# Optimization experiments

Hardware: AMD Instinct MI355X
Metric: run time of the kernel (lower is better)

## Reference

```python
import jax, jax.numpy as jnp
import numpy as np

B, C, H, W = 8, 256, 64, 64
NUM_HEADS = 4


def setup_inputs() -> dict:
    key = jax.random.key(0)
    ks = jax.random.split(key, 6)
    s = 0.02  # small init scale for 1x1 conv weights
    return {
        "x": jax.random.normal(ks[0], (B, C, H, W), jnp.float32),
        "cproj": jax.random.normal(ks[1], (B, C, H, W), jnp.float32),
        "wq": jax.random.normal(ks[2], (C, C), jnp.float32) * s,
        "bq": jnp.zeros((C,), jnp.float32),
        "wkv": jax.random.normal(ks[3], (2 * C, C), jnp.float32) * s,
        "bkv": jnp.zeros((2 * C,), jnp.float32),
        "wo": jax.random.normal(ks[4], (C, C), jnp.float32) * s,  # zero_module in torch; random here for a meaningful baseline
        "bo": jnp.zeros((C,), jnp.float32),
    }


def reference(x, cproj, wq, bq, wkv, bkv, wo, bo):
    Bb, Cc, Hh, Ww = x.shape
    N = Hh * Ww
    h = NUM_HEADS
    d = Cc // h
    scale = 1.0 / jnp.sqrt(jnp.sqrt(jnp.asarray(Cc, jnp.float32)))

    xf = x.reshape(Bb, Cc, N)
    cf = cproj.reshape(Bb, Cc, N)

    # 1x1 convs == channel matmuls
    Q = jnp.einsum('oc,bcn->bon', wq, xf) + bq[None, :, None]           # (B,C,N)
    KV = jnp.einsum('oc,bcn->bon', wkv, cf) + bkv[None, :, None]        # (B,2C,N)
    K, V = KV[:, :Cc], KV[:, Cc:]

    # softmax over channel-dim-within-head for q, over spatial N for k
    q = jax.nn.softmax(Q.reshape(Bb, h, d, N) * scale, axis=2).reshape(Bb, Cc, N)
    k = jax.nn.softmax(K.reshape(Bb, h, d, N), axis=3).reshape(Bb, Cc, N)

    # linear-attention: (B,C,C) context, then project back to N — note heads are mixed, per original bmm
    context = jnp.einsum('bcn,bdn->bcd', k, V)
    out = jnp.einsum('bcd,bdn->bcn', context, q)

    out = jnp.einsum('oc,bcn->bon', wo, out) + bo[None, :, None]
    return out.reshape(Bb, Cc, Hh, Ww)
```

## Files before the change

### kernel.cpp

```cpp
#include <hip/hip_runtime.h>

#define B_ 8
#define C_ 256
#define N_ 4096
#define NSPLIT 16

typedef float f32x4 __attribute__((ext_vector_type(4)));
typedef __bf16 bf16x8 __attribute__((ext_vector_type(8)));
typedef unsigned short u16x8 __attribute__((ext_vector_type(8)));
typedef unsigned short u16x4 __attribute__((ext_vector_type(4)));

__device__ __forceinline__ unsigned short f2bf(float f) {
  unsigned u = __float_as_uint(f);
  u += 0x7fff + ((u >> 16) & 1);
  return (unsigned short)(u >> 16);
}

__device__ __forceinline__ f32x4 mfma16(bf16x8 a, bf16x8 b, f32x4 c) {
  return __builtin_amdgcn_mfma_f32_16x16x32_bf16(a, b, c, 0, 0, 0);
}

typedef __attribute__((address_space(1))) const void* gvp;
typedef __attribute__((address_space(3))) void* lvp;
__device__ __forceinline__ void gld16(const void* g, void* l) {
  __builtin_amdgcn_global_load_lds((gvp)g, (lvp)l, 16, 0, 0);
}

template <int ROWS>
__device__ __forceinline__ void stage(unsigned short* lds, const unsigned short* g,
                                      int ld, int w, int lane) {
  const int r8 = lane >> 3;
  const int ce = ((lane & 7) ^ r8) << 3;
  const unsigned short* gp = g + (size_t)(w * (ROWS / 4) + r8) * ld + ce;
  unsigned short* lp = lds + w * (ROWS / 4) * 64;
#pragma unroll
  for (int i = 0; i < ROWS / 32; i++)
    gld16(gp + (size_t)(i * 8) * ld, lp + i * 512);
}

__device__ __forceinline__ bf16x8 frag(const unsigned short* lds, int row, int kc) {
  return *(const bf16x8*)(lds + row * 64 + ((kc ^ (row & 7)) << 3));
}

__device__ __forceinline__ void loadB(float4* pbv, const float* src, int ld,
                                      int n0, int kt, int w, int lane) {
  const int nf = lane & 15, kg = lane >> 4;
  const float* sp = src + (size_t)(kt * 64 + w * 16 + kg * 4) * ld + n0 + 4 * nf;
#pragma unroll
  for (int i = 0; i < 4; i++) pbv[i] = *(const float4*)(sp + (size_t)i * ld);
}
__device__ __forceinline__ void writeB(unsigned short* Bs, const float4* pbv,
                                       int w, int lane) {
  const int nf = lane & 15, kg = lane >> 4;
  const int k0 = w * 16 + kg * 4;
#pragma unroll
  for (int j = 0; j < 4; j++) {
    u16x4 o = (u16x4){f2bf(((const float*)&pbv[0])[j]), f2bf(((const float*)&pbv[1])[j]),
                      f2bf(((const float*)&pbv[2])[j]), f2bf(((const float*)&pbv[3])[j])};
    *(u16x4*)&Bs[(4 * nf + j) * 68 + k0] = o;
  }
}
__device__ __forceinline__ bf16x8 fragB(const unsigned short* Bs, int n, int k8) {
  union { u16x4 q[2]; bf16x8 b; } u;
  const unsigned short* p = Bs + n * 68 + k8 * 8;
  u.q[0] = *(const u16x4*)p;
  u.q[1] = *(const u16x4*)(p + 4);
  return u.b;
}

__global__ __launch_bounds__(256) void castw(
    const float* __restrict__ wq, const float* __restrict__ wkv,
    const float* __restrict__ wo, unsigned short* __restrict__ wqb,
    unsigned short* __restrict__ wkvb, unsigned short* __restrict__ wob) {
  int i = (blockIdx.x * 256 + threadIdx.x) * 4;
  const float* src;
  unsigned short* dst;
  int off;
  if (i < 65536) { src = wq; dst = wqb; off = i; }
  else if (i < 196608) { src = wkv; dst = wkvb; off = i - 65536; }
  else { src = wo; dst = wob; off = i - 196608; }
  float4 v = *(const float4*)(src + off);
  *(u16x4*)(dst + off) = (u16x4){f2bf(v.x), f2bf(v.y), f2bf(v.z), f2bf(v.w)};
}

__device__ __forceinline__ void qproj_body(
    unsigned short* As, unsigned short* Bs, const unsigned short* __restrict__ wqb,
    const float* __restrict__ x, const float* __restrict__ bq,
    unsigned short* __restrict__ qT, int b, int n0, int m0b) {
  const int tid = threadIdx.x, lane = tid & 63, w = tid >> 6;
  const int m0w = (w >> 1) * 64;
  const int n0w = (w & 1) * 32;
  const int colL = lane & 15, kq = lane >> 4, quad = lane >> 4;
  const float* xb = x + (size_t)b * C_ * N_;

  f32x4 acc[4][2];
#pragma unroll
  for (int i = 0; i < 4; i++)
#pragma unroll
    for (int j = 0; j < 2; j++) acc[i][j] = (f32x4){0.f, 0.f, 0.f, 0.f};

  float4 pbv[4];
  loadB(pbv, xb, N_, n0, 0, w, lane);

  for (int kt = 0; kt < 4; kt++) {
    writeB(Bs, pbv, w, lane);
    stage<128>(As, wqb + (size_t)m0b * C_ + kt * 64, C_, w, lane);
    __syncthreads();
    if (kt < 3) loadB(pbv, xb, N_, n0, kt + 1, w, lane);
#pragma unroll
    for (int ks = 0; ks < 2; ks++) {
      bf16x8 af[4], bf[2];
#pragma unroll
      for (int mt = 0; mt < 4; mt++) af[mt] = frag(As, m0w + mt * 16 + colL, ks * 4 + kq);
#pragma unroll
      for (int nt = 0; nt < 2; nt++) bf[nt] = fragB(Bs, n0w + nt * 16 + colL, ks * 4 + kq);
#pragma unroll
      for (int mt = 0; mt < 4; mt++)
#pragma unroll
        for (int nt = 0; nt < 2; nt++) acc[mt][nt] = mfma16(af[mt], bf[nt], acc[mt][nt]);
    }
    __syncthreads();
  }

#pragma unroll
  for (int nt = 0; nt < 2; nt++) {
    float v[16];
    float mx = -1e30f;
#pragma unroll
    for (int mt = 0; mt < 4; mt++)
#pragma unroll
      for (int r = 0; r < 4; r++) {
        int m = m0b + m0w + mt * 16 + quad * 4 + r;
        float val = (acc[mt][nt][r] + bq[m]) * 0.25f;
        v[mt * 4 + r] = val;
        mx = fmaxf(mx, val);
      }
    mx = fmaxf(mx, __shfl_xor(mx, 16));
    mx = fmaxf(mx, __shfl_xor(mx, 32));
    float s = 0.f;
#pragma unroll
    for (int j = 0; j < 16; j++) { v[j] = __expf(v[j] - mx); s += v[j]; }
    s += __shfl_xor(s, 16);
    s += __shfl_xor(s, 32);
    float inv = 1.0f / s;
    const int n = n0 + n0w + nt * 16 + colL;
    unsigned short* qb = qT + ((size_t)b * N_ + n) * C_ + m0b + m0w;
#pragma unroll
    for (int mt = 0; mt < 4; mt++) {
      u16x4 o = (u16x4){f2bf(v[mt * 4 + 0] * inv), f2bf(v[mt * 4 + 1] * inv),
                        f2bf(v[mt * 4 + 2] * inv), f2bf(v[mt * 4 + 3] * inv)};
      *(u16x4*)(qb + mt * 16 + quad * 4) = o;
    }
  }
}

__device__ __forceinline__ void kvproj_body(
    unsigned short* As, unsigned short* Bs, const unsigned short* __restrict__ wkvb,
    const float* __restrict__ cp, const float* __restrict__ bkv,
    float* __restrict__ Kf, unsigned short* __restrict__ Vb, int b, int n0, int m0b) {
  const int tid = threadIdx.x, lane = tid & 63, w = tid >> 6;
  const int m0w = w * 32;
  const int colL = lane & 15, kq = lane >> 4, quad = lane >> 4;
  const float* cpb = cp + (size_t)b * C_ * N_;

  f32x4 acc[2][4];
#pragma unroll
  for (int i = 0; i < 2; i++)
#pragma unroll
    for (int j = 0; j < 4; j++) acc[i][j] = (f32x4){0.f, 0.f, 0.f, 0.f};

  float4 pbv[4];
  loadB(pbv, cpb, N_, n0, 0, w, lane);

  for (int kt = 0; kt < 4; kt++) {
    writeB(Bs, pbv, w, lane);
    stage<128>(As, wkvb + (size_t)m0b * C_ + kt * 64, C_, w, lane);
    __syncthreads();
    if (kt < 3) loadB(pbv, cpb, N_, n0, kt + 1, w, lane);
#pragma unroll
    for (int ks = 0; ks < 2; ks++) {
      bf16x8 bf[4];
#pragma unroll
      for (int nt = 0; nt < 4; nt++) bf[nt] = fragB(Bs, nt * 16 + colL, ks * 4 + kq);
#pragma unroll
      for (int mt = 0; mt < 2; mt++) {
        bf16x8 af = frag(As, m0w + mt * 16 + colL, ks * 4 + kq);
#pragma unroll
        for (int nt = 0; nt < 4; nt++) acc[mt][nt] = mfma16(af, bf[nt], acc[mt][nt]);
      }
    }
    __syncthreads();
  }

#pragma unroll
  for (int mt = 0; mt < 2; mt++)
#pragma unroll
    for (int r = 0; r < 4; r++) {
      int m = m0b + m0w + mt * 16 + quad * 4 + r;
      float bias = bkv[m];
      if (m < C_) {
        float* kr = Kf + ((size_t)b * C_ + m) * N_ + n0;
#pragma unroll
        for (int nt = 0; nt < 4; nt++) kr[nt * 16 + colL] = acc[mt][nt][r] + bias;
      } else {
        unsigned short* vr = Vb + ((size_t)b * C_ + m - C_) * N_ + n0;
#pragma unroll
        for (int nt = 0; nt < 4; nt++) vr[nt * 16 + colL] = f2bf(acc[mt][nt][r] + bias);
      }
    }
}

__global__ __launch_bounds__(256) void qkvproj(
    const unsigned short* __restrict__ wqb, const unsigned short* __restrict__ wkvb,
    const float* __restrict__ x, const float* __restrict__ cp,
    const float* __restrict__ bq, const float* __restrict__ bkv,
    unsigned short* __restrict__ qT, float* __restrict__ Kf,
    unsigned short* __restrict__ Vb) {
  __shared__ __align__(16) unsigned short As[128 * 64];
  __shared__ __align__(16) unsigned short Bs[64 * 68];
  const int b = blockIdx.z, n0 = blockIdx.x * 64;
  if (blockIdx.y < 2)
    qproj_body(As, Bs, wqb, x, bq, qT, b, n0, blockIdx.y * 128);
  else
    kvproj_body(As, Bs, wkvb, cp, bkv, Kf, Vb, b, n0, (blockIdx.y - 2) * 128);
}

__global__ __launch_bounds__(256) void ksoftmax(const float* __restrict__ Kf,
                                                unsigned short* __restrict__ kb) {
  const int b = blockIdx.x >> 8, c = blockIdx.x & 255;
  const float* row = Kf + ((size_t)b * C_ + c) * N_;
  unsigned short* orow = kb + ((size_t)b * C_ + c) * N_;
  const int t = threadIdx.x, lane = t & 63, wv = t >> 6;
  __shared__ float red[8];

  float4 v[4];
  float mx = -1e30f;
#pragma unroll
  for (int i = 0; i < 4; i++) {
    v[i] = *(const float4*)&row[i * 1024 + t * 4];
    mx = fmaxf(fmaxf(fmaxf(mx, v[i].x), fmaxf(v[i].y, v[i].z)), v[i].w);
  }
#pragma unroll
  for (int o = 32; o > 0; o >>= 1) mx = fmaxf(mx, __shfl_down(mx, o));
  if (lane == 0) red[wv] = mx;
  __syncthreads();
  mx = fmaxf(fmaxf(red[0], red[1]), fmaxf(red[2], red[3]));

  float s = 0.f;
#pragma unroll
  for (int i = 0; i < 4; i++) {
    v[i].x = __expf(v[i].x - mx); v[i].y = __expf(v[i].y - mx);
    v[i].z = __expf(v[i].z - mx); v[i].w = __expf(v[i].w - mx);
    s += v[i].x + v[i].y + v[i].z + v[i].w;
  }
#pragma unroll
  for (int o = 32; o > 0; o >>= 1) s += __shfl_down(s, o);
  if (lane == 0) red[4 + wv] = s;
  __syncthreads();
  float inv = 1.0f / (red[4] + red[5] + red[6] + red[7]);
#pragma unroll
  for (int i = 0; i < 4; i++) {
    u16x4 o = (u16x4){f2bf(v[i].x * inv), f2bf(v[i].y * inv),
                      f2bf(v[i].z * inv), f2bf(v[i].w * inv)};
    *(u16x4*)&orow[i * 1024 + t * 4] = o;
  }
}

__global__ __launch_bounds__(256) void ctx_part(
    const unsigned short* __restrict__ kb, const unsigned short* __restrict__ Vb,
    float* __restrict__ ctxp) {
  __shared__ __align__(16) unsigned short As[128 * 64];
  __shared__ __align__(16) unsigned short Bs[64 * 64];
  const int z = blockIdx.z, b = z >> 4, s = z & 15;
  const int m0 = blockIdx.y * 128, n0 = blockIdx.x * 64;
  const int tid = threadIdx.x, lane = tid & 63, w = tid >> 6;
  const int m0w = (w & 1) * 64, n0w = (w >> 1) * 32;
  const int colL = lane & 15, kq = lane >> 4, quad = lane >> 4;
  const unsigned short* Ag = kb + ((size_t)b * C_ + m0) * N_;
  const unsigned short* Bg = Vb + ((size_t)b * C_ + n0) * N_;
  const int kbeg = s * (N_ / NSPLIT);

  f32x4 acc[4][2];
#pragma unroll
  for (int i = 0; i < 4; i++)
#pragma unroll
    for (int j = 0; j < 2; j++) acc[i][j] = (f32x4){0.f, 0.f, 0.f, 0.f};

  for (int kt = 0; kt < (N_ / NSPLIT) / 64; kt++) {
    stage<128>(As, Ag + kbeg + kt * 64, N_, w, lane);
    stage<64>(Bs, Bg + kbeg + kt * 64, N_, w, lane);
    __syncthreads();
#pragma unroll
    for (int ks = 0; ks < 2; ks++) {
      bf16x8 af[4], bf[2];
#pragma unroll
      for (int mt = 0; mt < 4; mt++) af[mt] = frag(As, m0w + mt * 16 + colL, ks * 4 + kq);
#pragma unroll
      for (int nt = 0; nt < 2; nt++) bf[nt] = frag(Bs, n0w + nt * 16 + colL, ks * 4 + kq);
#pragma unroll
      for (int mt = 0; mt < 4; mt++)
#pragma unroll
        for (int nt = 0; nt < 2; nt++) acc[mt][nt] = mfma16(af[mt], bf[nt], acc[mt][nt]);
    }
    __syncthreads();
  }

  float* outp = ctxp + ((size_t)s * B_ + b) * C_ * C_;
#pragma unroll
  for (int mt = 0; mt < 4; mt++)
#pragma unroll
    for (int nt = 0; nt < 2; nt++)
#pragma unroll
      for (int r = 0; r < 4; r++) {
        int m = m0 + m0w + mt * 16 + quad * 4 + r;
        int n = n0 + n0w + nt * 16 + colL;
        outp[(size_t)m * C_ + n] = acc[mt][nt][r];
      }
}

__global__ __launch_bounds__(256) void ctx_reduce_t(const float* __restrict__ ctxp,
                                                    unsigned short* __restrict__ ctxsT) {
  __shared__ unsigned short t[64][72];
  const int b = blockIdx.z, c0 = blockIdx.y * 64, d0 = blockIdx.x * 64;
  const int tid = threadIdx.x;
  const int cl = tid >> 2, dg = (tid & 3) * 16;
  const float* base = ctxp + ((size_t)b * C_ + c0 + cl) * C_ + d0 + dg;
  float acc[16];
#pragma unroll
  for (int j = 0; j < 16; j++) acc[j] = 0.f;
  for (int s = 0; s < NSPLIT; s++) {
    const float* p = base + (size_t)s * B_ * C_ * C_;
#pragma unroll
    for (int j = 0; j < 16; j += 4) {
      float4 v = *(const float4*)(p + j);
      acc[j] += v.x; acc[j + 1] += v.y; acc[j + 2] += v.z; acc[j + 3] += v.w;
    }
  }
#pragma unroll
  for (int j = 0; j < 16; j++) t[dg + j][cl] = f2bf(acc[j]);
  __syncthreads();
  const int dr = tid >> 2, cg = (tid & 3) * 16;
  unsigned short* dp = ctxsT + ((size_t)b * C_ + d0 + dr) * C_ + c0 + cg;
  *(u16x8*)dp = *(const u16x8*)&t[dr][cg];
  *(u16x8*)(dp + 8) = *(const u16x8*)&t[dr][cg + 8];
}

__global__ __launch_bounds__(256) void oproj(
    const unsigned short* __restrict__ wob, const unsigned short* __restrict__ ctxsT,
    unsigned short* __restrict__ ctx2) {
  __shared__ __align__(16) unsigned short As[64 * 64];
  __shared__ __align__(16) unsigned short Bs[64 * 64];
  const int b = blockIdx.z, m0 = blockIdx.y * 64, n0 = blockIdx.x * 64;
  const int tid = threadIdx.x, lane = tid & 63, w = tid >> 6;
  const int m0w = (w & 1) * 32, n0w = (w >> 1) * 32;
  const int colL = lane & 15, kq = lane >> 4, quad = lane >> 4;
  const unsigned short* Ag = wob + (size_t)m0 * C_;
  const unsigned short* Bg = ctxsT + ((size_t)b * C_ + n0) * C_;

  f32x4 acc[2][2];
#pragma unroll
  for (int i = 0; i < 2; i++)
#pragma unroll
    for (int j = 0; j < 2; j++) acc[i][j] = (f32x4){0.f, 0.f, 0.f, 0.f};

  for (int kt = 0; kt < 4; kt++) {
    stage<64>(As, Ag + kt * 64, C_, w, lane);
    stage<64>(Bs, Bg + kt * 64, C_, w, lane);
    __syncthreads();
#pragma unroll
    for (int ks = 0; ks < 2; ks++) {
      bf16x8 af[2], bf[2];
#pragma unroll
      for (int mt = 0; mt < 2; mt++) af[mt] = frag(As, m0w + mt * 16 + colL, ks * 4 + kq);
#pragma unroll
      for (int nt = 0; nt < 2; nt++) bf[nt] = frag(Bs, n0w + nt * 16 + colL, ks * 4 + kq);
#pragma unroll
      for (int mt = 0; mt < 2; mt++)
#pragma unroll
        for (int nt = 0; nt < 2; nt++) acc[mt][nt] = mfma16(af[mt], bf[nt], acc[mt][nt]);
    }
    __syncthreads();
  }

  unsigned short* ob = ctx2 + (size_t)b * C_ * C_;
#pragma unroll
  for (int mt = 0; mt < 2; mt++)
#pragma unroll
    for (int nt = 0; nt < 2; nt++)
#pragma unroll
      for (int r = 0; r < 4; r++) {
        int m = m0 + m0w + mt * 16 + quad * 4 + r;
        int n = n0 + n0w + nt * 16 + colL;
        ob[(size_t)m * C_ + n] = f2bf(acc[mt][nt][r]);
      }
}

__global__ __launch_bounds__(256) void outgemm(
    const unsigned short* __restrict__ ctx2, const unsigned short* __restrict__ qT,
    const float* __restrict__ bo, float* __restrict__ out) {
  __shared__ __align__(16) unsigned short As[128 * 64];
  __shared__ __align__(16) unsigned short Bs[64 * 64];
  const int b = blockIdx.z, n0 = blockIdx.x * 64, m0b = blockIdx.y * 128;
  const int tid = threadIdx.x, lane = tid & 63, w = tid >> 6;
  const int m0w = w * 32;
  const int colL = lane & 15, kq = lane >> 4, quad = lane >> 4;
  const unsigned short* Ag = ctx2 + (size_t)b * C_ * C_ + (size_t)m0b * C_;
  const unsigned short* Bg = qT + ((size_t)b * N_ + n0) * C_;

  f32x4 acc[2][4];
#pragma unroll
  for (int i = 0; i < 2; i++)
#pragma unroll
    for (int j = 0; j < 4; j++) acc[i][j] = (f32x4){0.f, 0.f, 0.f, 0.f};

  for (int kt = 0; kt < 4; kt++) {
    stage<128>(As, Ag + kt * 64, C_, w, lane);
    stage<64>(Bs, Bg + kt * 64, C_, w, lane);
    __syncthreads();
#pragma unroll
    for (int ks = 0; ks < 2; ks++) {
      bf16x8 af[2], bf[4];
#pragma unroll
      for (int mt = 0; mt < 2; mt++) af[mt] = frag(As, m0w + mt * 16 + colL, ks * 4 + kq);
#pragma unroll
      for (int nt = 0; nt < 4; nt++) bf[nt] = frag(Bs, nt * 16 + colL, ks * 4 + kq);
#pragma unroll
      for (int mt = 0; mt < 2; mt++)
#pragma unroll
        for (int nt = 0; nt < 4; nt++) acc[mt][nt] = mfma16(af[mt], bf[nt], acc[mt][nt]);
    }
    __syncthreads();
  }

  float* ob = out + (size_t)b * C_ * N_;
#pragma unroll
  for (int mt = 0; mt < 2; mt++)
#pragma unroll
    for (int r = 0; r < 4; r++) {
      int m = m0b + m0w + mt * 16 + quad * 4 + r;
      float bias = bo[m];
#pragma unroll
      for (int nt = 0; nt < 4; nt++) {
        int n = n0 + nt * 16 + colL;
        ob[(size_t)m * N_ + n] = acc[mt][nt][r] + bias;
      }
    }
}

extern "C" void kernel_launch(void* const* d_in, const int* in_sizes, int n_in,
                              void* d_out, int out_size, void* d_ws, size_t ws_size,
                              hipStream_t stream) {
  const float* x     = (const float*)d_in[0];
  const float* cproj = (const float*)d_in[1];
  const float* wq    = (const float*)d_in[2];
  const float* bq    = (const float*)d_in[3];
  const float* wkv   = (const float*)d_in[4];
  const float* bkv   = (const float*)d_in[5];
  const float* wo    = (const float*)d_in[6];
  const float* bo    = (const float*)d_in[7];
  float* out = (float*)d_out;

  unsigned short* qT    = (unsigned short*)d_ws;
  float*          Kf    = (float*)(qT + 8388608);
  unsigned short* Vb    = (unsigned short*)(Kf + 8388608);
  unsigned short* kb    = Vb + 8388608;
  float*          ctxp  = (float*)(kb + 8388608);
  unsigned short* wqb   = (unsigned short*)(ctxp + 8388608);
  unsigned short* wkvb  = wqb + 65536;
  unsigned short* wob   = wkvb + 131072;
  unsigned short* ctxsT = wob + 65536;
  unsigned short* ctx2  = ctxsT + 524288;

  castw<<<256, 256, 0, stream>>>(wq, wkv, wo, wqb, wkvb, wob);
  qkvproj<<<dim3(64, 6, 8), 256, 0, stream>>>(wqb, wkvb, x, cproj, bq, bkv, qT, Kf, Vb);
  ksoftmax<<<2048, 256, 0, stream>>>(Kf, kb);
  ctx_part<<<dim3(4, 2, 128), 256, 0, stream>>>(kb, Vb, ctxp);
  ctx_reduce_t<<<dim3(4, 4, 8), 256, 0, stream>>>(ctxp, ctxsT);
  oproj<<<dim3(4, 4, 8), 256, 0, stream>>>(wob, ctxsT, ctx2);
  outgemm<<<dim3(64, 2, 8), 256, 0, stream>>>(ctx2, qT, bo, out);
}
```

Measured before the change: 199.1 us.

## Double-buffer LDS tiles in all GEMM kernels to overlap loads with MFMA

Shared-memory A/B tiles in the qkv projection, context, oproj and output GEMMs are now two-deep ping-pong buffers. Two K-tiles are preloaded before the loop. The tile for step kt+2 is issued into the freed buffer right after the compute of step kt, so global loads overlap the MFMA work of the next step. This aims to hide global-to-LDS latency, which is exposed because each block has few K iterations. In exchange, LDS use per block roughly doubles, which can lower occupancy. The qkv path also adds an extra barrier per iteration.

```diff
diff --git a/kernel.cpp b/kernel.cpp
--- a/kernel.cpp
+++ b/kernel.cpp
@@ -84,14 +84,16 @@
 }
 
 __device__ __forceinline__ void qproj_body(
-    unsigned short* As, unsigned short* Bs, const unsigned short* __restrict__ wqb,
-    const float* __restrict__ x, const float* __restrict__ bq,
-    unsigned short* __restrict__ qT, int b, int n0, int m0b) {
+    unsigned short (*As)[128 * 64], unsigned short (*Bs)[64 * 68],
+    const unsigned short* __restrict__ wqb, const float* __restrict__ x,
+    const float* __restrict__ bq, unsigned short* __restrict__ qT,
+    int b, int n0, int m0b) {
   const int tid = threadIdx.x, lane = tid & 63, w = tid >> 6;
   const int m0w = (w >> 1) * 64;
   const int n0w = (w & 1) * 32;
   const int colL = lane & 15, kq = lane >> 4, quad = lane >> 4;
   const float* xb = x + (size_t)b * C_ * N_;
+  const unsigned short* wg = wqb + (size_t)m0b * C_;
 
   f32x4 acc[4][2];
 #pragma unroll
@@ -101,25 +103,36 @@
 
   float4 pbv[4];
   loadB(pbv, xb, N_, n0, 0, w, lane);
+  stage<128>(As[0], wg + 0 * 64, C_, w, lane);
+  writeB(Bs[0], pbv, w, lane);
+  loadB(pbv, xb, N_, n0, 1, w, lane);
+  stage<128>(As[1], wg + 1 * 64, C_, w, lane);
+  __syncthreads();
 
   for (int kt = 0; kt < 4; kt++) {
-    writeB(Bs, pbv, w, lane);
-    stage<128>(As, wqb + (size_t)m0b * C_ + kt * 64, C_, w, lane);
-    __syncthreads();
-    if (kt < 3) loadB(pbv, xb, N_, n0, kt + 1, w, lane);
+    const unsigned short* Asc = As[kt & 1];
+    const unsigned short* Bsc = Bs[kt & 1];
 #pragma unroll
     for (int ks = 0; ks < 2; ks++) {
       bf16x8 af[4], bf[2];
 #pragma unroll
-      for (int mt = 0; mt < 4; mt++) af[mt] = frag(As, m0w + mt * 16 + colL, ks * 4 + kq);
-#pragma unroll
-      for (int nt = 0; nt < 2; nt++) bf[nt] = fragB(Bs, n0w + nt * 16 + colL, ks * 4 + kq);
+      for (int mt = 0; mt < 4; mt++) af[mt] = frag(Asc, m0w + mt * 16 + colL, ks * 4 + kq);
+#pragma unroll
+      for (int nt = 0; nt < 2; nt++) bf[nt] = fragB(Bsc, n0w + nt * 16 + colL, ks * 4 + kq);
 #pragma unroll
       for (int mt = 0; mt < 4; mt++)
 #pragma unroll
         for (int nt = 0; nt < 2; nt++) acc[mt][nt] = mfma16(af[mt], bf[nt], acc[mt][nt]);
     }
     __syncthreads();
+    if (kt < 3) {
+      writeB(Bs[(kt + 1) & 1], pbv, w, lane);
+      __syncthreads();
+      if (kt < 2) {
+        stage<128>(As[kt & 1], wg + (kt + 2) * 64, C_, w, lane);
+        loadB(pbv, xb, N_, n0, kt + 2, w, lane);
+      }
+    }
   }
 
 #pragma unroll
@@ -155,13 +168,15 @@
 }
 
 __device__ __forceinline__ void kvproj_body(
-    unsigned short* As, unsigned short* Bs, const unsigned short* __restrict__ wkvb,
-    const float* __restrict__ cp, const float* __restrict__ bkv,
-    float* __restrict__ Kf, unsigned short* __restrict__ Vb, int b, int n0, int m0b) {
+    unsigned short (*As)[128 * 64], unsigned short (*Bs)[64 * 68],
+    const unsigned short* __restrict__ wkvb, const float* __restrict__ cp,
+    const float* __restrict__ bkv, float* __restrict__ Kf,
+    unsigned short* __restrict__ Vb, int b, int n0, int m0b) {
   const int tid = threadIdx.x, lane = tid & 63, w = tid >> 6;
   const int m0w = w * 32;
   const int colL = lane & 15, kq = lane >> 4, quad = lane >> 4;
   const float* cpb = cp + (size_t)b * C_ * N_;
+  const unsigned short* wg = wkvb + (size_t)m0b * C_;
 
   f32x4 acc[2][4];
 #pragma unroll
@@ -171,25 +186,36 @@
 
   float4 pbv[4];
   loadB(pbv, cpb, N_, n0, 0, w, lane);
+  stage<128>(As[0], wg + 0 * 64, C_, w, lane);
+  writeB(Bs[0], pbv, w, lane);
+  loadB(pbv, cpb, N_, n0, 1, w, lane);
+  stage<128>(As[1], wg + 1 * 64, C_, w, lane);
+  __syncthreads();
 
   for (int kt = 0; kt < 4; kt++) {
-    writeB(Bs, pbv, w, lane);
-    stage<128>(As, wkvb + (size_t)m0b * C_ + kt * 64, C_, w, lane);
-    __syncthreads();
-    if (kt < 3) loadB(pbv, cpb, N_, n0, kt + 1, w, lane);
+    const unsigned short* Asc = As[kt & 1];
+    const unsigned short* Bsc = Bs[kt & 1];
 #pragma unroll
     for (int ks = 0; ks < 2; ks++) {
       bf16x8 bf[4];
 #pragma unroll
-      for (int nt = 0; nt < 4; nt++) bf[nt] = fragB(Bs, nt * 16 + colL, ks * 4 + kq);
+      for (int nt = 0; nt < 4; nt++) bf[nt] = fragB(Bsc, nt * 16 + colL, ks * 4 + kq);
 #pragma unroll
       for (int mt = 0; mt < 2; mt++) {
-        bf16x8 af = frag(As, m0w + mt * 16 + colL, ks * 4 + kq);
+        bf16x8 af = frag(Asc, m0w + mt * 16 + colL, ks * 4 + kq);
 #pragma unroll
         for (int nt = 0; nt < 4; nt++) acc[mt][nt] = mfma16(af, bf[nt], acc[mt][nt]);
       }
     }
     __syncthreads();
+    if (kt < 3) {
+      writeB(Bs[(kt + 1) & 1], pbv, w, lane);
+      __syncthreads();
+      if (kt < 2) {
+        stage<128>(As[kt & 1], wg + (kt + 2) * 64, C_, w, lane);
+        loadB(pbv, cpb, N_, n0, kt + 2, w, lane);
+      }
+    }
   }
 
 #pragma unroll
@@ -216,8 +242,8 @@
     const float* __restrict__ bq, const float* __restrict__ bkv,
     unsigned short* __restrict__ qT, float* __restrict__ Kf,
     unsigned short* __restrict__ Vb) {
-  __shared__ __align__(16) unsigned short As[128 * 64];
-  __shared__ __align__(16) unsigned short Bs[64 * 68];
+  __shared__ __align__(16) unsigned short As[2][128 * 64];
+  __shared__ __align__(16) unsigned short Bs[2][64 * 68];
   const int b = blockIdx.z, n0 = blockIdx.x * 64;
   if (blockIdx.y < 2)
     qproj_body(As, Bs, wqb, x, bq, qT, b, n0, blockIdx.y * 128);
@@ -269,8 +295,8 @@
 __global__ __launch_bounds__(256) void ctx_part(
     const unsigned short* __restrict__ kb, const unsigned short* __restrict__ Vb,
     float* __restrict__ ctxp) {
-  __shared__ __align__(16) unsigned short As[128 * 64];
-  __shared__ __align__(16) unsigned short Bs[64 * 64];
+  __shared__ __align__(16) unsigned short As[2][128 * 64];
+  __shared__ __align__(16) unsigned short Bs[2][64 * 64];
   const int z = blockIdx.z, b = z >> 4, s = z & 15;
   const int m0 = blockIdx.y * 128, n0 = blockIdx.x * 64;
   const int tid = threadIdx.x, lane = tid & 63, w = tid >> 6;
@@ -279,6 +305,7 @@
   const unsigned short* Ag = kb + ((size_t)b * C_ + m0) * N_;
   const unsigned short* Bg = Vb + ((size_t)b * C_ + n0) * N_;
   const int kbeg = s * (N_ / NSPLIT);
+  const int NK = (N_ / NSPLIT) / 64;
 
   f32x4 acc[4][2];
 #pragma unroll
@@ -286,23 +313,32 @@
 #pragma unroll
     for (int j = 0; j < 2; j++) acc[i][j] = (f32x4){0.f, 0.f, 0.f, 0.f};
 
-  for (int kt = 0; kt < (N_ / NSPLIT) / 64; kt++) {
-    stage<128>(As, Ag + kbeg + kt * 64, N_, w, lane);
-    stage<64>(Bs, Bg + kbeg + kt * 64, N_, w, lane);
-    __syncthreads();
+  stage<128>(As[0], Ag + kbeg + 0 * 64, N_, w, lane);
+  stage<64>(Bs[0], Bg + kbeg + 0 * 64, N_, w, lane);
+  stage<128>(As[1], Ag + kbeg + 1 * 64, N_, w, lane);
+  stage<64>(Bs[1], Bg + kbeg + 1 * 64, N_, w, lane);
+  __syncthreads();
+
+  for (int kt = 0; kt < NK; kt++) {
+    const unsigned short* Asc = As[kt & 1];
+    const unsigned short* Bsc = Bs[kt & 1];
 #pragma unroll
     for (int ks = 0; ks < 2; ks++) {
       bf16x8 af[4], bf[2];
 #pragma unroll
-      for (int mt = 0; mt < 4; mt++) af[mt] = frag(As, m0w + mt * 16 + colL, ks * 4 + kq);
-#pragma unroll
-      for (int nt = 0; nt < 2; nt++) bf[nt] = frag(Bs, n0w + nt * 16 + colL, ks * 4 + kq);
+      for (int mt = 0; mt < 4; mt++) af[mt] = frag(Asc, m0w + mt * 16 + colL, ks * 4 + kq);
+#pragma unroll
+      for (int nt = 0; nt < 2; nt++) bf[nt] = frag(Bsc, n0w + nt * 16 + colL, ks * 4 + kq);
 #pragma unroll
       for (int mt = 0; mt < 4; mt++)
 #pragma unroll
         for (int nt = 0; nt < 2; nt++) acc[mt][nt] = mfma16(af[mt], bf[nt], acc[mt][nt]);
     }
     __syncthreads();
+    if (kt + 2 < NK) {
+      stage<128>(As[kt & 1], Ag + kbeg + (kt + 2) * 64, N_, w, lane);
+      stage<64>(Bs[kt & 1], Bg + kbeg + (kt + 2) * 64, N_, w, lane);
+    }
   }
 
   float* outp = ctxp + ((size_t)s * B_ + b) * C_ * C_;
@@ -348,8 +384,8 @@
 __global__ __launch_bounds__(256) void oproj(
     const unsigned short* __restrict__ wob, const unsigned short* __restrict__ ctxsT,
     unsigned short* __restrict__ ctx2) {
-  __shared__ __align__(16) unsigned short As[64 * 64];
-  __shared__ __align__(16) unsigned short Bs[64 * 64];
+  __shared__ __align__(16) unsigned short As[2][64 * 64];
+  __shared__ __align__(16) unsigned short Bs[2][64 * 64];
   const int b = blockIdx.z, m0 = blockIdx.y * 64, n0 = blockIdx.x * 64;
   const int tid = threadIdx.x, lane = tid & 63, w = tid >> 6;
   const int m0w = (w & 1) * 32, n0w = (w >> 1) * 32;
@@ -363,23 +399,32 @@
 #pragma unroll
     for (int j = 0; j < 2; j++) acc[i][j] = (f32x4){0.f, 0.f, 0.f, 0.f};
 
+  stage<64>(As[0], Ag + 0 * 64, C_, w, lane);
+  stage<64>(Bs[0], Bg + 0 * 64, C_, w, lane);
+  stage<64>(As[1], Ag + 1 * 64, C_, w, lane);
+  stage<64>(Bs[1], Bg + 1 * 64, C_, w, lane);
+  __syncthreads();
+
   for (int kt = 0; kt < 4; kt++) {
-    stage<64>(As, Ag + kt * 64, C_, w, lane);
-    stage<64>(Bs, Bg + kt * 64, C_, w, lane);
-    __syncthreads();
+    const unsigned short* Asc = As[kt & 1];
+    const unsigned short* Bsc = Bs[kt & 1];
 #pragma unroll
     for (int ks = 0; ks < 2; ks++) {
       bf16x8 af[2], bf[2];
 #pragma unroll
-      for (int mt = 0; mt < 2; mt++) af[mt] = frag(As, m0w + mt * 16 + colL, ks * 4 + kq);
-#pragma unroll
-      for (int nt = 0; nt < 2; nt++) bf[nt] = frag(Bs, n0w + nt * 16 + colL, ks * 4 + kq);
+      for (int mt = 0; mt < 2; mt++) af[mt] = frag(Asc, m0w + mt * 16 + colL, ks * 4 + kq);
+#pragma unroll
+      for (int nt = 0; nt < 2; nt++) bf[nt] = frag(Bsc, n0w + nt * 16 + colL, ks * 4 + kq);
 #pragma unroll
       for (int mt = 0; mt < 2; mt++)
 #pragma unroll
         for (int nt = 0; nt < 2; nt++) acc[mt][nt] = mfma16(af[mt], bf[nt], acc[mt][nt]);
     }
     __syncthreads();
+    if (kt + 2 < 4) {
+      stage<64>(As[kt & 1], Ag + (kt + 2) * 64, C_, w, lane);
+      stage<64>(Bs[kt & 1], Bg + (kt + 2) * 64, C_, w, lane);
+    }
   }
 
   unsigned short* ob = ctx2 + (size_t)b * C_ * C_;
@@ -398,8 +443,8 @@
 __global__ __launch_bounds__(256) void outgemm(
     const unsigned short* __restrict__ ctx2, const unsigned short* __restrict__ qT,
     const float* __restrict__ bo, float* __restrict__ out) {
-  __shared__ __align__(16) unsigned short As[128 * 64];
-  __shared__ __align__(16) unsigned short Bs[64 * 64];
+  __shared__ __align__(16) unsigned short As[2][128 * 64];
+  __shared__ __align__(16) unsigned short Bs[2][64 * 64];
   const int b = blockIdx.z, n0 = blockIdx.x * 64, m0b = blockIdx.y * 128;
   const int tid = threadIdx.x, lane = tid & 63, w = tid >> 6;
   const int m0w = w * 32;
@@ -413,23 +458,32 @@
 #pragma unroll
     for (int j = 0; j < 4; j++) acc[i][j] = (f32x4){0.f, 0.f, 0.f, 0.f};
 
+  stage<128>(As[0], Ag + 0 * 64, C_, w, lane);
+  stage<64>(Bs[0], Bg + 0 * 64, C_, w, lane);
+  stage<128>(As[1], Ag + 1 * 64, C_, w, lane);
+  stage<64>(Bs[1], Bg + 1 * 64, C_, w, lane);
+  __syncthreads();
+
   for (int kt = 0; kt < 4; kt++) {
-    stage<128>(As, Ag + kt * 64, C_, w, lane);
-    stage<64>(Bs, Bg + kt * 64, C_, w, lane);
-    __syncthreads();
+    const unsigned short* Asc = As[kt & 1];
+    const unsigned short* Bsc = Bs[kt & 1];
 #pragma unroll
     for (int ks = 0; ks < 2; ks++) {
       bf16x8 af[2], bf[4];
 #pragma unroll
-      for (int mt = 0; mt < 2; mt++) af[mt] = frag(As, m0w + mt * 16 + colL, ks * 4 + kq);
-#pragma unroll
-      for (int nt = 0; nt < 4; nt++) bf[nt] = frag(Bs, nt * 16 + colL, ks * 4 + kq);
+      for (int mt = 0; mt < 2; mt++) af[mt] = frag(Asc, m0w + mt * 16 + colL, ks * 4 + kq);
+#pragma unroll
+      for (int nt = 0; nt < 4; nt++) bf[nt] = frag(Bsc, nt * 16 + colL, ks * 4 + kq);
 #pragma unroll
       for (int mt = 0; mt < 2; mt++)
 #pragma unroll
         for (int nt = 0; nt < 4; nt++) acc[mt][nt] = mfma16(af[mt], bf[nt], acc[mt][nt]);
     }
     __syncthreads();
+    if (kt + 2 < 4) {
+      stage<128>(As[kt & 1], Ag + (kt + 2) * 64, C_, w, lane);
+      stage<64>(Bs[kt & 1], Bg + (kt + 2) * 64, C_, w, lane);
+    }
   }
 
   float* ob = out + (size_t)b * C_ * N_;
```

Result: slower. 205.2 us (+3.0%).

## Fuse K softmax into projection and context kernels; merge reduce with output projection

Applied to the files above, without the earlier changes.

Removes the standalone K softmax pass. The kv projection now accumulates per-row exp sums into a zeroed buffer with atomics, and the context GEMM loads fp32 K directly, applying exp and the 1/Z normalization while staging into LDS. It also fuses the split-K context reduction with the Wo projection into one kernel, which drops the transposed intermediate buffer and one launch. In exchange, max subtraction is dropped from the softmax, which risks overflow for large logits. The context GEMM also reads fp32 K instead of bf16 and recomputes exp there.

```diff
diff --git a/kernel.cpp b/kernel.cpp
--- a/kernel.cpp
+++ b/kernel.cpp
@@ -68,11 +68,22 @@
   return u.b;
 }
 
+__device__ __forceinline__ bf16x8 fragC(const unsigned short* Ct, int n, int k8) {
+  union { u16x4 q[2]; bf16x8 b; } u;
+  const unsigned short* p = Ct + n * 268 + k8 * 8;
+  u.q[0] = *(const u16x4*)p;
+  u.q[1] = *(const u16x4*)(p + 4);
+  return u.b;
+}
+
 __global__ __launch_bounds__(256) void castw(
     const float* __restrict__ wq, const float* __restrict__ wkv,
     const float* __restrict__ wo, unsigned short* __restrict__ wqb,
-    unsigned short* __restrict__ wkvb, unsigned short* __restrict__ wob) {
-  int i = (blockIdx.x * 256 + threadIdx.x) * 4;
+    unsigned short* __restrict__ wkvb, unsigned short* __restrict__ wob,
+    float* __restrict__ Z) {
+  int t = blockIdx.x * 256 + threadIdx.x;
+  if (t < B_ * C_) Z[t] = 0.f;
+  int i = t * 4;
   const float* src;
   unsigned short* dst;
   int off;
@@ -157,7 +168,8 @@
 __device__ __forceinline__ void kvproj_body(
     unsigned short* As, unsigned short* Bs, const unsigned short* __restrict__ wkvb,
     const float* __restrict__ cp, const float* __restrict__ bkv,
-    float* __restrict__ Kf, unsigned short* __restrict__ Vb, int b, int n0, int m0b) {
+    float* __restrict__ Kf, unsigned short* __restrict__ Vb,
+    float* __restrict__ Z, int b, int n0, int m0b) {
   const int tid = threadIdx.x, lane = tid & 63, w = tid >> 6;
   const int m0w = w * 32;
   const int colL = lane & 15, kq = lane >> 4, quad = lane >> 4;
@@ -200,8 +212,18 @@
       float bias = bkv[m];
       if (m < C_) {
         float* kr = Kf + ((size_t)b * C_ + m) * N_ + n0;
-#pragma unroll
-        for (int nt = 0; nt < 4; nt++) kr[nt * 16 + colL] = acc[mt][nt][r] + bias;
+        float es = 0.f;
+#pragma unroll
+        for (int nt = 0; nt < 4; nt++) {
+          float vv = acc[mt][nt][r] + bias;
+          kr[nt * 16 + colL] = vv;
+          es += __expf(vv);
+        }
+        es += __shfl_xor(es, 1);
+        es += __shfl_xor(es, 2);
+        es += __shfl_xor(es, 4);
+        es += __shfl_xor(es, 8);
+        if ((lane & 15) == 0) atomicAdd(&Z[b * C_ + m], es);
       } else {
         unsigned short* vr = Vb + ((size_t)b * C_ + m - C_) * N_ + n0;
 #pragma unroll
@@ -215,60 +237,19 @@
     const float* __restrict__ x, const float* __restrict__ cp,
     const float* __restrict__ bq, const float* __restrict__ bkv,
     unsigned short* __restrict__ qT, float* __restrict__ Kf,
-    unsigned short* __restrict__ Vb) {
+    unsigned short* __restrict__ Vb, float* __restrict__ Z) {
   __shared__ __align__(16) unsigned short As[128 * 64];
   __shared__ __align__(16) unsigned short Bs[64 * 68];
   const int b = blockIdx.z, n0 = blockIdx.x * 64;
   if (blockIdx.y < 2)
     qproj_body(As, Bs, wqb, x, bq, qT, b, n0, blockIdx.y * 128);
   else
-    kvproj_body(As, Bs, wkvb, cp, bkv, Kf, Vb, b, n0, (blockIdx.y - 2) * 128);
-}
-
-__global__ __launch_bounds__(256) void ksoftmax(const float* __restrict__ Kf,
-                                                unsigned short* __restrict__ kb) {
-  const int b = blockIdx.x >> 8, c = blockIdx.x & 255;
-  const float* row = Kf + ((size_t)b * C_ + c) * N_;
-  unsigned short* orow = kb + ((size_t)b * C_ + c) * N_;
-  const int t = threadIdx.x, lane = t & 63, wv = t >> 6;
-  __shared__ float red[8];
-
-  float4 v[4];
-  float mx = -1e30f;
-#pragma unroll
-  for (int i = 0; i < 4; i++) {
-    v[i] = *(const float4*)&row[i * 1024 + t * 4];
-    mx = fmaxf(fmaxf(fmaxf(mx, v[i].x), fmaxf(v[i].y, v[i].z)), v[i].w);
-  }
-#pragma unroll
-  for (int o = 32; o > 0; o >>= 1) mx = fmaxf(mx, __shfl_down(mx, o));
-  if (lane == 0) red[wv] = mx;
-  __syncthreads();
-  mx = fmaxf(fmaxf(red[0], red[1]), fmaxf(red[2], red[3]));
-
-  float s = 0.f;
-#pragma unroll
-  for (int i = 0; i < 4; i++) {
-    v[i].x = __expf(v[i].x - mx); v[i].y = __expf(v[i].y - mx);
-    v[i].z = __expf(v[i].z - mx); v[i].w = __expf(v[i].w - mx);
-    s += v[i].x + v[i].y + v[i].z + v[i].w;
-  }
-#pragma unroll
-  for (int o = 32; o > 0; o >>= 1) s += __shfl_down(s, o);
-  if (lane == 0) red[4 + wv] = s;
-  __syncthreads();
-  float inv = 1.0f / (red[4] + red[5] + red[6] + red[7]);
-#pragma unroll
-  for (int i = 0; i < 4; i++) {
-    u16x4 o = (u16x4){f2bf(v[i].x * inv), f2bf(v[i].y * inv),
-                      f2bf(v[i].z * inv), f2bf(v[i].w * inv)};
-    *(u16x4*)&orow[i * 1024 + t * 4] = o;
-  }
+    kvproj_body(As, Bs, wkvb, cp, bkv, Kf, Vb, Z, b, n0, (blockIdx.y - 2) * 128);
 }
 
 __global__ __launch_bounds__(256) void ctx_part(
-    const unsigned short* __restrict__ kb, const unsigned short* __restrict__ Vb,
-    float* __restrict__ ctxp) {
+    const float* __restrict__ Kf, const float* __restrict__ Z,
+    const unsigned short* __restrict__ Vb, float* __restrict__ ctxp) {
   __shared__ __align__(16) unsigned short As[128 * 64];
   __shared__ __align__(16) unsigned short Bs[64 * 64];
   const int z = blockIdx.z, b = z >> 4, s = z & 15;
@@ -276,10 +257,13 @@
   const int tid = threadIdx.x, lane = tid & 63, w = tid >> 6;
   const int m0w = (w & 1) * 64, n0w = (w >> 1) * 32;
   const int colL = lane & 15, kq = lane >> 4, quad = lane >> 4;
-  const unsigned short* Ag = kb + ((size_t)b * C_ + m0) * N_;
-  const unsigned short* Bg = Vb + ((size_t)b * C_ + n0) * N_;
   const int kbeg = s * (N_ / NSPLIT);
 
+  const int arow = tid >> 1, ahalf = tid & 1;
+  const float* akf = Kf + ((size_t)b * C_ + m0 + arow) * N_ + kbeg + ahalf * 32;
+  const float invz = 1.0f / Z[b * C_ + m0 + arow];
+  const unsigned short* Bg = Vb + ((size_t)b * C_ + n0) * N_ + kbeg;
+
   f32x4 acc[4][2];
 #pragma unroll
   for (int i = 0; i < 4; i++)
@@ -287,8 +271,18 @@
     for (int j = 0; j < 2; j++) acc[i][j] = (f32x4){0.f, 0.f, 0.f, 0.f};
 
   for (int kt = 0; kt < (N_ / NSPLIT) / 64; kt++) {
-    stage<128>(As, Ag + kbeg + kt * 64, N_, w, lane);
-    stage<64>(Bs, Bg + kbeg + kt * 64, N_, w, lane);
+    stage<64>(Bs, Bg + kt * 64, N_, w, lane);
+#pragma unroll
+    for (int j = 0; j < 4; j++) {
+      float4 a0 = *(const float4*)(akf + kt * 64 + j * 8);
+      float4 a1 = *(const float4*)(akf + kt * 64 + j * 8 + 4);
+      const int c8 = ahalf * 4 + j;
+      u16x8 o = (u16x8){f2bf(__expf(a0.x) * invz), f2bf(__expf(a0.y) * invz),
+                        f2bf(__expf(a0.z) * invz), f2bf(__expf(a0.w) * invz),
+                        f2bf(__expf(a1.x) * invz), f2bf(__expf(a1.y) * invz),
+                        f2bf(__expf(a1.z) * invz), f2bf(__expf(a1.w) * invz)};
+      *(u16x8*)&As[arow * 64 + ((c8 ^ (arow & 7)) << 3)] = o;
+    }
     __syncthreads();
 #pragma unroll
     for (int ks = 0; ks < 2; ks++) {
@@ -318,81 +312,57 @@
       }
 }
 
-__global__ __launch_bounds__(256) void ctx_reduce_t(const float* __restrict__ ctxp,
-                                                    unsigned short* __restrict__ ctxsT) {
-  __shared__ unsigned short t[64][72];
-  const int b = blockIdx.z, c0 = blockIdx.y * 64, d0 = blockIdx.x * 64;
-  const int tid = threadIdx.x;
-  const int cl = tid >> 2, dg = (tid & 3) * 16;
-  const float* base = ctxp + ((size_t)b * C_ + c0 + cl) * C_ + d0 + dg;
-  float acc[16];
-#pragma unroll
-  for (int j = 0; j < 16; j++) acc[j] = 0.f;
-  for (int s = 0; s < NSPLIT; s++) {
-    const float* p = base + (size_t)s * B_ * C_ * C_;
-#pragma unroll
-    for (int j = 0; j < 16; j += 4) {
-      float4 v = *(const float4*)(p + j);
-      acc[j] += v.x; acc[j + 1] += v.y; acc[j + 2] += v.z; acc[j + 3] += v.w;
-    }
-  }
-#pragma unroll
-  for (int j = 0; j < 16; j++) t[dg + j][cl] = f2bf(acc[j]);
+__global__ __launch_bounds__(256) void ctxoproj(
+    const float* __restrict__ ctxp, const unsigned short* __restrict__ wob,
+    unsigned short* __restrict__ ctx2) {
+  __shared__ __align__(16) unsigned short AsW[4 * 64 * 64];
+  __shared__ __align__(16) unsigned short Ct[32 * 268];
+  const int b = blockIdx.z, o0 = blockIdx.y * 64, d0 = blockIdx.x * 32;
+  const int tid = threadIdx.x, lane = tid & 63, w = tid >> 6;
+  const int colL = lane & 15, kq = lane >> 4, quad = lane >> 4;
+
+#pragma unroll
+  for (int ck = 0; ck < 4; ck++)
+    stage<64>(AsW + ck * 4096, wob + (size_t)o0 * C_ + ck * 64, C_, w, lane);
+
+  const int q = tid & 7, cl = tid >> 3;
+  const float* pb = ctxp + ((size_t)b * C_ + cl) * C_ + d0 + q * 4;
+#pragma unroll 2
+  for (int p = 0; p < 8; p++) {
+    f32x4 s4 = (f32x4){0.f, 0.f, 0.f, 0.f};
+    const float* pp = pb + (size_t)p * 32 * C_;
+#pragma unroll
+    for (int s = 0; s < NSPLIT; s++) {
+      float4 v = *(const float4*)(pp + (size_t)s * B_ * C_ * C_);
+      s4[0] += v.x; s4[1] += v.y; s4[2] += v.z; s4[3] += v.w;
+    }
+    const int c = p * 32 + cl;
+#pragma unroll
+    for (int j = 0; j < 4; j++) Ct[(q * 4 + j) * 268 + c] = f2bf(s4[j]);
+  }
   __syncthreads();
-  const int dr = tid >> 2, cg = (tid & 3) * 16;
-  unsigned short* dp = ctxsT + ((size_t)b * C_ + d0 + dr) * C_ + c0 + cg;
-  *(u16x8*)dp = *(const u16x8*)&t[dr][cg];
-  *(u16x8*)(dp + 8) = *(const u16x8*)&t[dr][cg + 8];
-}
-
-__global__ __launch_bounds__(256) void oproj(
-    const unsigned short* __restrict__ wob, const unsigned short* __restrict__ ctxsT,
-    unsigned short* __restrict__ ctx2) {
-  __shared__ __align__(16) unsigned short As[64 * 64];
-  __shared__ __align__(16) unsigned short Bs[64 * 64];
-  const int b = blockIdx.z, m0 = blockIdx.y * 64, n0 = blockIdx.x * 64;
-  const int tid = threadIdx.x, lane = tid & 63, w = tid >> 6;
-  const int m0w = (w & 1) * 32, n0w = (w >> 1) * 32;
-  const int colL = lane & 15, kq = lane >> 4, quad = lane >> 4;
-  const unsigned short* Ag = wob + (size_t)m0 * C_;
-  const unsigned short* Bg = ctxsT + ((size_t)b * C_ + n0) * C_;
-
-  f32x4 acc[2][2];
-#pragma unroll
-  for (int i = 0; i < 2; i++)
-#pragma unroll
-    for (int j = 0; j < 2; j++) acc[i][j] = (f32x4){0.f, 0.f, 0.f, 0.f};
-
-  for (int kt = 0; kt < 4; kt++) {
-    stage<64>(As, Ag + kt * 64, C_, w, lane);
-    stage<64>(Bs, Bg + kt * 64, C_, w, lane);
-    __syncthreads();
+
+  f32x4 acc2[2];
+  acc2[0] = (f32x4){0.f, 0.f, 0.f, 0.f};
+  acc2[1] = (f32x4){0.f, 0.f, 0.f, 0.f};
+#pragma unroll
+  for (int kt = 0; kt < 4; kt++)
 #pragma unroll
     for (int ks = 0; ks < 2; ks++) {
-      bf16x8 af[2], bf[2];
-#pragma unroll
-      for (int mt = 0; mt < 2; mt++) af[mt] = frag(As, m0w + mt * 16 + colL, ks * 4 + kq);
-#pragma unroll
-      for (int nt = 0; nt < 2; nt++) bf[nt] = frag(Bs, n0w + nt * 16 + colL, ks * 4 + kq);
-#pragma unroll
-      for (int mt = 0; mt < 2; mt++)
-#pragma unroll
-        for (int nt = 0; nt < 2; nt++) acc[mt][nt] = mfma16(af[mt], bf[nt], acc[mt][nt]);
-    }
-    __syncthreads();
-  }
-
+      bf16x8 af = frag(AsW + kt * 4096, w * 16 + colL, ks * 4 + kq);
+#pragma unroll
+      for (int nt = 0; nt < 2; nt++) {
+        bf16x8 bf = fragC(Ct, nt * 16 + colL, kt * 8 + ks * 4 + kq);
+        acc2[nt] = mfma16(af, bf, acc2[nt]);
+      }
+    }
   unsigned short* ob = ctx2 + (size_t)b * C_ * C_;
 #pragma unroll
-  for (int mt = 0; mt < 2; mt++)
-#pragma unroll
-    for (int nt = 0; nt < 2; nt++)
-#pragma unroll
-      for (int r = 0; r < 4; r++) {
-        int m = m0 + m0w + mt * 16 + quad * 4 + r;
-        int n = n0 + n0w + nt * 16 + colL;
-        ob[(size_t)m * C_ + n] = f2bf(acc[mt][nt][r]);
-      }
+  for (int nt = 0; nt < 2; nt++)
+#pragma unroll
+    for (int r = 0; r < 4; r++)
+      ob[(size_t)(o0 + w * 16 + quad * 4 + r) * C_ + d0 + nt * 16 + colL] =
+          f2bf(acc2[nt][r]);
 }
 
 __global__ __launch_bounds__(256) void outgemm(
@@ -463,19 +433,17 @@
   unsigned short* qT    = (unsigned short*)d_ws;
   float*          Kf    = (float*)(qT + 8388608);
   unsigned short* Vb    = (unsigned short*)(Kf + 8388608);
-  unsigned short* kb    = Vb + 8388608;
-  float*          ctxp  = (float*)(kb + 8388608);
+  float*          ctxp  = (float*)(Vb + 8388608);
   unsigned short* wqb   = (unsigned short*)(ctxp + 8388608);
   unsigned short* wkvb  = wqb + 65536;
   unsigned short* wob   = wkvb + 131072;
-  unsigned short* ctxsT = wob + 65536;
-  unsigned short* ctx2  = ctxsT + 524288;
-
-  castw<<<256, 256, 0, stream>>>(wq, wkv, wo, wqb, wkvb, wob);
-  qkvproj<<<dim3(64, 6, 8), 256, 0, stream>>>(wqb, wkvb, x, cproj, bq, bkv, qT, Kf, Vb);
-  ksoftmax<<<2048, 256, 0, stream>>>(Kf, kb);
-  ctx_part<<<dim3(4, 2, 128), 256, 0, stream>>>(kb, Vb, ctxp);
-  ctx_reduce_t<<<dim3(4, 4, 8), 256, 0, stream>>>(ctxp, ctxsT);
-  oproj<<<dim3(4, 4, 8), 256, 0, stream>>>(wob, ctxsT, ctx2);
+  unsigned short* ctx2  = wob + 65536;
+  float*          Zbuf  = (float*)(ctx2 + 524288);
+
+  castw<<<256, 256, 0, stream>>>(wq, wkv, wo, wqb, wkvb, wob, Zbuf);
+  qkvproj<<<dim3(64, 6, 8), 256, 0, stream>>>(wqb, wkvb, x, cproj, bq, bkv,
+                                              qT, Kf, Vb, Zbuf);
+  ctx_part<<<dim3(4, 2, 128), 256, 0, stream>>>(Kf, Zbuf, Vb, ctxp);
+  ctxoproj<<<dim3(8, 4, 8), 256, 0, stream>>>(ctxp, wob, ctx2);
   outgemm<<<dim3(64, 2, 8), 256, 0, stream>>>(ctx2, qT, bo, out);
 }
```

Result: slower. 212.0 us (+6.5%).
